# Kernel tuning notes

Hardware: AMD Instinct MI355X
Metric: run time of the kernel (lower is better)

Reference implementation:

```python
import jax, jax.numpy as jnp
import numpy as np

WIN = 5                # win_size
DT = (WIN - 1) // 2    # delta_t
OUT_DIM = 64


def setup_inputs() -> dict:
    key = jax.random.key(0)
    k1, k2, k3 = jax.random.split(key, 3)
    N, C, J, T = 64, 16, 25, 120
    c = C + 1                      # + time channel (signatory.Augment include_time=True)
    sig_ch = c + c * c             # signature_channels(c, depth=2)
    x = jax.random.normal(k1, (N, C, J, T), jnp.float32)
    W = jax.random.normal(k2, (sig_ch, OUT_DIM), jnp.float32) * 0.05
    b = jax.random.normal(k3, (OUT_DIM,), jnp.float32) * 0.05
    return {"x": x, "W": W, "b": b}


def _window_increments(x):
    # Boundary windows are shorter (clip); we emulate them by clipping indices so
    # out-of-range slots duplicate the endpoint -> zero increments -> identity in
    # the tensor algebra, leaving the signature unchanged (faithful to the ragged loop).
    N, C, J, T = x.shape
    t = jnp.arange(T)
    pos = t[:, None] + (jnp.arange(WIN) - DT)[None, :]
    start = jnp.maximum(t - DT, 0)
    end = jnp.minimum(t + DT + 1, T)
    L = (end - start).astype(jnp.float32)                     # window length, >= DT+1
    pc = jnp.clip(pos, 0, T - 1)
    xp = jnp.transpose(x, (0, 2, 3, 1))                       # [N,J,T,C]
    pts = xp[:, :, pc, :]
    # signatory time channel = linspace(0,1,L) over the valid window;
    # duplicated boundary slots share the endpoint's time (zero increment)
    time = (pc - start[:, None]).astype(jnp.float32) / (L[:, None] - 1.0)
    time_b = jnp.broadcast_to(time[None, None, :, :, None], (N, J, T, WIN, 1))
    path = jnp.concatenate([pts, time_b], axis=-1)
    path = jnp.concatenate([jnp.zeros_like(path[..., :1, :]), path], axis=-2)  # basepoint=True
    return jnp.diff(path, axis=-2)


def _signature_depth2(inc):
    c = inc.shape[-1]
    lead = inc.shape[:-2]
    S1 = jnp.zeros(lead + (c,), inc.dtype)
    S2 = jnp.zeros(lead + (c, c), inc.dtype)

    def step(carry, v):
        S1, S2 = carry
        S2 = S2 + S1[..., :, None] * v[..., None, :] + 0.5 * (v[..., :, None] * v[..., None, :])
        S1 = S1 + v
        return (S1, S2), None

    (S1, S2), _ = jax.lax.scan(step, (S1, S2), jnp.moveaxis(inc, -2, 0))
    return S1, S2


def reference(x, W, b):
    inc = _window_increments(x)
    S1, S2 = _signature_depth2(inc)                           # [N,J,T,c], [N,J,T,c,c]
    y = jnp.concatenate([S1, S2.reshape(S2.shape[:-2] + (-1,))], axis=-1)  # [N,J,T,306]
    z = jnp.einsum('njts,so->njto', y, W) + b                 # Linear
    return jnp.transpose(z, (0, 3, 1, 2))                     # [N,out_dim,J,T]
```

## Files before the change

### kernel.cpp

```cpp
#include <hip/hip_runtime.h>
#include <hip/hip_fp16.h>

#define J_DIM 25
#define T_DIM 120
#define O_DIM 64
#define KPAD  328
#define TB    64
#define WROWS 68
#define XPADH 24

typedef _Float16 f16x8 __attribute__((ext_vector_type(8)));
typedef __attribute__((ext_vector_type(4))) float f32x4;

__device__ __forceinline__ unsigned h2bits(__half2 h) {
    unsigned u; __builtin_memcpy(&u, &h, 4); return u;
}
__device__ __forceinline__ __half2 bits2h(unsigned u) {
    __half2 h; __builtin_memcpy(&h, &u, 4); return h;
}
__device__ __forceinline__ __half2 sel4h(int q, __half2 a, __half2 b, __half2 c, __half2 d) {
    unsigned s01 = (q & 1) ? h2bits(b) : h2bits(a);
    unsigned s23 = (q & 1) ? h2bits(d) : h2bits(c);
    return bits2h((q & 2) ? s23 : s01);
}

__global__ void wprep(const float* __restrict__ W, __half* __restrict__ Wf) {
    int i = blockIdx.x * 256 + threadIdx.x;
    if (i >= O_DIM * KPAD) return;
    int o = i / KPAD, k = i % KPAD;
    int a = k / 18, b = k % 18;
    float v = 0.0f;
    if (k < 306) v = (b == 17) ? W[a * O_DIM + o] : 0.5f * W[(17 + 17 * a + b) * O_DIM + o];
    Wf[o * KPAD + k] = __float2half(v);
}

__global__ __launch_bounds__(256, 2) void sig_mfma(
    const float* __restrict__ x, const __half* __restrict__ Wf,
    const float* __restrict__ bias, float* __restrict__ out)
{
    __shared__ __half xs[WROWS][XPADH];
    __shared__ __half ys[TB * KPAD];

    const int tid = threadIdx.x;
    const int bid = blockIdx.x;
    const int half_ = bid & 1;
    const int j = (bid >> 1) % J_DIM;
    const int n = bid / (2 * J_DIM);
    const int t0 = half_ * 56;
    const int wave = tid >> 6, lane = tid & 63;
    const int l15 = lane & 15, l4 = lane >> 4;

    const float* xbase = x + ((size_t)(n * 16) * J_DIM + j) * T_DIM;
    for (int idx = tid; idx < 16 * WROWS; idx += 256) {
        int c = idx / WROWS, i = idx % WROWS;
        int st = min(max(t0 - 2 + i, 0), T_DIM - 1);
        xs[i][c] = __float2half(xbase[(size_t)c * J_DIM * T_DIM + st]);
    }
    if (tid < TB * 3) {
        int r = tid / 3, p = tid % 3;
        *(uint4*)((char*)ys + r * 656 + 608 + p * 16) = uint4{0, 0, 0, 0};
    }
    __syncthreads();

    {
        const int row = tid >> 2, qg = tid & 3;
        const int t = t0 + row;
        const int start = max(t - 2, 0), end = min(t + 3, T_DIM);
        const float inv = 1.0f / (float)(end - start - 1);
        float ptvf[5];
        #pragma unroll
        for (int w = 0; w < 5; ++w) {
            int pcw = min(max(t - 2 + w, 0), T_DIM - 1);
            ptvf[w] = (float)(pcw - start) * inv;
        }
        __half2 ptvb[5];
        #pragma unroll
        for (int w = 0; w < 5; ++w) ptvb[w] = __float2half2_rn(ptvf[w]);

        __half2 xw[5][8];
        #pragma unroll
        for (int w = 0; w < 5; ++w) {
            uint4 lo = *(const uint4*)&xs[row + w][0];
            uint4 hi = *(const uint4*)&xs[row + w][8];
            xw[w][0] = bits2h(lo.x); xw[w][1] = bits2h(lo.y);
            xw[w][2] = bits2h(lo.z); xw[w][3] = bits2h(lo.w);
            xw[w][4] = bits2h(hi.x); xw[w][5] = bits2h(hi.y);
            xw[w][6] = bits2h(hi.z); xw[w][7] = bits2h(hi.w);
        }

        {
            __half2 pr[5];
            #pragma unroll
            for (int w = 0; w < 5; ++w)
                pr[w] = sel4h(qg, xw[w][0], xw[w][1], xw[w][2], xw[w][3]);
            __half2 hp[5];
            hp[0] = __hneg2(pr[1]);
            hp[1] = __hsub2(pr[0], pr[2]);
            hp[2] = __hsub2(pr[1], pr[3]);
            hp[3] = __hsub2(pr[2], pr[4]);
            hp[4] = __hadd2(pr[3], pr[4]);
            __half2 h0b[5], h1b[5];
            #pragma unroll
            for (int w = 0; w < 5; ++w) {
                h0b[w] = __low2half2(hp[w]);
                h1b[w] = __high2half2(hp[w]);
            }
            unsigned u0[9], u1[9];
            #pragma unroll
            for (int b2 = 0; b2 < 8; ++b2) {
                __half2 a0 = __hmul2(h0b[0], xw[0][b2]);
                __half2 a1 = __hmul2(h1b[0], xw[0][b2]);
                #pragma unroll
                for (int w = 1; w < 5; ++w) {
                    a0 = __hfma2(h0b[w], xw[w][b2], a0);
                    a1 = __hfma2(h1b[w], xw[w][b2], a1);
                }
                u0[b2] = h2bits(a0);
                u1[b2] = h2bits(a1);
            }
            {
                __half2 a16 = __hmul2(hp[0], ptvb[0]);
                #pragma unroll
                for (int w = 1; w < 5; ++w) a16 = __hfma2(hp[w], ptvb[w], a16);
                u0[8] = h2bits(__halves2half2(__low2half(a16),  __low2half(pr[4])));
                u1[8] = h2bits(__halves2half2(__high2half(a16), __high2half(pr[4])));
            }
            char* yr = (char*)ys + row * 656 + 72 * qg;
            *(uint2*)(yr +  0) = uint2{u0[0], u0[1]};
            *(uint2*)(yr +  8) = uint2{u0[2], u0[3]};
            *(uint2*)(yr + 16) = uint2{u0[4], u0[5]};
            *(uint2*)(yr + 24) = uint2{u0[6], u0[7]};
            *(uint2*)(yr + 32) = uint2{u0[8], u1[0]};
            *(uint2*)(yr + 40) = uint2{u1[1], u1[2]};
            *(uint2*)(yr + 48) = uint2{u1[3], u1[4]};
            *(uint2*)(yr + 56) = uint2{u1[5], u1[6]};
            *(uint2*)(yr + 64) = uint2{u1[7], u1[8]};
        }

        {
            __half2 pr[5];
            #pragma unroll
            for (int w = 0; w < 5; ++w)
                pr[w] = sel4h(qg, xw[w][4], xw[w][5], xw[w][6], xw[w][7]);
            __half2 hp[5];
            hp[0] = __hneg2(pr[1]);
            hp[1] = __hsub2(pr[0], pr[2]);
            hp[2] = __hsub2(pr[1], pr[3]);
            hp[3] = __hsub2(pr[2], pr[4]);
            hp[4] = __hadd2(pr[3], pr[4]);
            __half2 h0b[5], h1b[5];
            #pragma unroll
            for (int w = 0; w < 5; ++w) {
                h0b[w] = __low2half2(hp[w]);
                h1b[w] = __high2half2(hp[w]);
            }
            unsigned u0[9], u1[9];
            #pragma unroll
            for (int b2 = 0; b2 < 8; ++b2) {
                __half2 a0 = __hmul2(h0b[0], xw[0][b2]);
                __half2 a1 = __hmul2(h1b[0], xw[0][b2]);
                #pragma unroll
                for (int w = 1; w < 5; ++w) {
                    a0 = __hfma2(h0b[w], xw[w][b2], a0);
                    a1 = __hfma2(h1b[w], xw[w][b2], a1);
                }
                u0[b2] = h2bits(a0);
                u1[b2] = h2bits(a1);
            }
            {
                __half2 a16 = __hmul2(hp[0], ptvb[0]);
                #pragma unroll
                for (int w = 1; w < 5; ++w) a16 = __hfma2(hp[w], ptvb[w], a16);
                u0[8] = h2bits(__halves2half2(__low2half(a16),  __low2half(pr[4])));
                u1[8] = h2bits(__halves2half2(__high2half(a16), __high2half(pr[4])));
            }
            char* yr = (char*)ys + row * 656 + 72 * qg + 288;
            *(uint2*)(yr +  0) = uint2{u0[0], u0[1]};
            *(uint2*)(yr +  8) = uint2{u0[2], u0[3]};
            *(uint2*)(yr + 16) = uint2{u0[4], u0[5]};
            *(uint2*)(yr + 24) = uint2{u0[6], u0[7]};
            *(uint2*)(yr + 32) = uint2{u0[8], u1[0]};
            *(uint2*)(yr + 40) = uint2{u1[1], u1[2]};
            *(uint2*)(yr + 48) = uint2{u1[3], u1[4]};
            *(uint2*)(yr + 56) = uint2{u1[5], u1[6]};
            *(uint2*)(yr + 64) = uint2{u1[7], u1[8]};
        }

        if (qg == 0) {
            __half2 htb[5];
            htb[0] = __float2half2_rn(-ptvf[1]);
            htb[1] = __float2half2_rn(ptvf[0] - ptvf[2]);
            htb[2] = __float2half2_rn(ptvf[1] - ptvf[3]);
            htb[3] = __float2half2_rn(ptvf[2] - ptvf[4]);
            htb[4] = __float2half2_rn(ptvf[3] + ptvf[4]);
            unsigned ut[9];
            #pragma unroll
            for (int b2 = 0; b2 < 8; ++b2) {
                __half2 a = __hmul2(htb[0], xw[0][b2]);
                #pragma unroll
                for (int w = 1; w < 5; ++w) a = __hfma2(htb[w], xw[w][b2], a);
                ut[b2] = h2bits(a);
            }
            {
                __half2 a = __hmul2(htb[0], ptvb[0]);
                #pragma unroll
                for (int w = 1; w < 5; ++w) a = __hfma2(htb[w], ptvb[w], a);
                ut[8] = h2bits(__halves2half2(__low2half(a), __float2half(ptvf[4])));
            }
            char* yt = (char*)ys + row * 656 + 576;
            *(uint2*)(yt +  0) = uint2{ut[0], ut[1]};
            *(uint2*)(yt +  8) = uint2{ut[2], ut[3]};
            *(uint2*)(yt + 16) = uint2{ut[4], ut[5]};
            *(uint2*)(yt + 24) = uint2{ut[6], ut[7]};
            *(unsigned*)(yt + 32) = ut[8];
        }
    }
    __syncthreads();

    {
        const float bv = bias[wave * 16 + l15];
        const __half* Bb = Wf + (size_t)(wave * 16 + l15) * KPAD + l4 * 8;
        f16x8 bfrag[10];
        #pragma unroll
        for (int kk = 0; kk < 10; ++kk)
            bfrag[kk] = *(const f16x8*)(Bb + kk * 32);
        #pragma unroll
        for (int mi = 0; mi < 4; ++mi) {
            const char* Ab = (const char*)ys + (mi * 16 + l15) * 656 + l4 * 16;
            f32x4 acc = f32x4{bv, bv, bv, bv};
            #pragma unroll
            for (int kk = 0; kk < 10; ++kk) {
                f16x8 af = *(const f16x8*)(Ab + kk * 64);
                acc = __builtin_amdgcn_mfma_f32_16x16x32_f16(af, bfrag[kk], acc, 0, 0, 0);
            }
            const int tg = t0 + mi * 16 + l4 * 4;
            float* op = out + ((size_t)(n * O_DIM + wave * 16 + l15) * J_DIM + j) * T_DIM + tg;
            *(f32x4*)op = acc;
        }
    }
}

extern "C" void kernel_launch(void* const* d_in, const int* in_sizes, int n_in,
                              void* d_out, int out_size, void* d_ws, size_t ws_size,
                              hipStream_t stream) {
    const float* x = (const float*)d_in[0];
    const float* W = (const float*)d_in[1];
    const float* b = (const float*)d_in[2];
    float* out = (float*)d_out;
    __half* Wf = (__half*)d_ws;

    wprep<<<(O_DIM * KPAD + 255) / 256, 256, 0, stream>>>(W, Wf);
    sig_mfma<<<64 * J_DIM * 2, 256, 0, stream>>>(x, Wf, b, out);
}
```

Before: 39.16 us.

## Make each wave independent with private LDS tiles and wave barriers

Each wave now loads its own 20-row x slice and builds a 16-row signature tile in a private LDS region. The block-wide __syncthreads calls become wave barriers. The MFMA stage is restructured so each wave keeps its A fragments in registers and loops over the four output-column groups, reading W fragments from global memory inside the loop. This removes cross-wave synchronisation and lets waves overlap, but each wave re-reads overlapping x rows and the whole of W.

```diff
diff --git a/kernel.cpp b/kernel.cpp
--- a/kernel.cpp
+++ b/kernel.cpp
@@ -5,8 +5,6 @@
 #define T_DIM 120
 #define O_DIM 64
 #define KPAD  328
-#define TB    64
-#define WROWS 68
 #define XPADH 24
 
 typedef _Float16 f16x8 __attribute__((ext_vector_type(8)));
@@ -38,33 +36,35 @@
     const float* __restrict__ x, const __half* __restrict__ Wf,
     const float* __restrict__ bias, float* __restrict__ out)
 {
-    __shared__ __half xs[WROWS][XPADH];
-    __shared__ __half ys[TB * KPAD];
+    __shared__ __half xs[4][20][XPADH];
+    __shared__ __half ys[4][16 * KPAD];
 
     const int tid = threadIdx.x;
+    const int wave = tid >> 6, lane = tid & 63;
+    const int l15 = lane & 15, l4 = lane >> 4;
     const int bid = blockIdx.x;
     const int half_ = bid & 1;
     const int j = (bid >> 1) % J_DIM;
     const int n = bid / (2 * J_DIM);
-    const int t0 = half_ * 56;
-    const int wave = tid >> 6, lane = tid & 63;
-    const int l15 = lane & 15, l4 = lane >> 4;
+    const int t0w = half_ * 56 + wave * 16;
 
     const float* xbase = x + ((size_t)(n * 16) * J_DIM + j) * T_DIM;
-    for (int idx = tid; idx < 16 * WROWS; idx += 256) {
-        int c = idx / WROWS, i = idx % WROWS;
-        int st = min(max(t0 - 2 + i, 0), T_DIM - 1);
-        xs[i][c] = __float2half(xbase[(size_t)c * J_DIM * T_DIM + st]);
-    }
-    if (tid < TB * 3) {
-        int r = tid / 3, p = tid % 3;
-        *(uint4*)((char*)ys + r * 656 + 608 + p * 16) = uint4{0, 0, 0, 0};
-    }
-    __syncthreads();
+    #pragma unroll
+    for (int k = 0; k < 5; ++k) {
+        int idx = lane + k * 64;
+        int c = idx / 20, i = idx % 20;
+        int st = min(max(t0w - 2 + i, 0), T_DIM - 1);
+        xs[wave][i][c] = __float2half(xbase[(size_t)c * J_DIM * T_DIM + st]);
+    }
+    if (lane < 32) {
+        int r = lane >> 1, p = lane & 1;
+        *(uint4*)((char*)&ys[wave][0] + r * 656 + 608 + p * 16) = uint4{0, 0, 0, 0};
+    }
+    __builtin_amdgcn_wave_barrier();
 
     {
-        const int row = tid >> 2, qg = tid & 3;
-        const int t = t0 + row;
+        const int row = lane >> 2, qg = lane & 3;
+        const int t = t0w + row;
         const int start = max(t - 2, 0), end = min(t + 3, T_DIM);
         const float inv = 1.0f / (float)(end - start - 1);
         float ptvf[5];
@@ -80,8 +80,8 @@
         __half2 xw[5][8];
         #pragma unroll
         for (int w = 0; w < 5; ++w) {
-            uint4 lo = *(const uint4*)&xs[row + w][0];
-            uint4 hi = *(const uint4*)&xs[row + w][8];
+            uint4 lo = *(const uint4*)&xs[wave][row + w][0];
+            uint4 hi = *(const uint4*)&xs[wave][row + w][8];
             xw[w][0] = bits2h(lo.x); xw[w][1] = bits2h(lo.y);
             xw[w][2] = bits2h(lo.z); xw[w][3] = bits2h(lo.w);
             xw[w][4] = bits2h(hi.x); xw[w][5] = bits2h(hi.y);
@@ -125,7 +125,7 @@
                 u0[8] = h2bits(__halves2half2(__low2half(a16),  __low2half(pr[4])));
                 u1[8] = h2bits(__halves2half2(__high2half(a16), __high2half(pr[4])));
             }
-            char* yr = (char*)ys + row * 656 + 72 * qg;
+            char* yr = (char*)&ys[wave][0] + row * 656 + 72 * qg;
             *(uint2*)(yr +  0) = uint2{u0[0], u0[1]};
             *(uint2*)(yr +  8) = uint2{u0[2], u0[3]};
             *(uint2*)(yr + 16) = uint2{u0[4], u0[5]};
@@ -174,7 +174,7 @@
                 u0[8] = h2bits(__halves2half2(__low2half(a16),  __low2half(pr[4])));
                 u1[8] = h2bits(__halves2half2(__high2half(a16), __high2half(pr[4])));
             }
-            char* yr = (char*)ys + row * 656 + 72 * qg + 288;
+            char* yr = (char*)&ys[wave][0] + row * 656 + 72 * qg + 288;
             *(uint2*)(yr +  0) = uint2{u0[0], u0[1]};
             *(uint2*)(yr +  8) = uint2{u0[2], u0[3]};
             *(uint2*)(yr + 16) = uint2{u0[4], u0[5]};
@@ -207,7 +207,7 @@
                 for (int w = 1; w < 5; ++w) a = __hfma2(htb[w], ptvb[w], a);
                 ut[8] = h2bits(__halves2half2(__low2half(a), __float2half(ptvf[4])));
             }
-            char* yt = (char*)ys + row * 656 + 576;
+            char* yt = (char*)&ys[wave][0] + row * 656 + 576;
             *(uint2*)(yt +  0) = uint2{ut[0], ut[1]};
             *(uint2*)(yt +  8) = uint2{ut[2], ut[3]};
             *(uint2*)(yt + 16) = uint2{ut[4], ut[5]};
@@ -215,26 +215,26 @@
             *(unsigned*)(yt + 32) = ut[8];
         }
     }
-    __syncthreads();
+    __builtin_amdgcn_wave_barrier();
 
     {
-        const float bv = bias[wave * 16 + l15];
-        const __half* Bb = Wf + (size_t)(wave * 16 + l15) * KPAD + l4 * 8;
-        f16x8 bfrag[10];
+        const char* Ab = (const char*)&ys[wave][0] + l15 * 656 + l4 * 16;
+        f16x8 af[10];
         #pragma unroll
         for (int kk = 0; kk < 10; ++kk)
-            bfrag[kk] = *(const f16x8*)(Bb + kk * 32);
-        #pragma unroll
-        for (int mi = 0; mi < 4; ++mi) {
-            const char* Ab = (const char*)ys + (mi * 16 + l15) * 656 + l4 * 16;
+            af[kk] = *(const f16x8*)(Ab + kk * 64);
+        const int tg = t0w + l4 * 4;
+        #pragma unroll
+        for (int c = 0; c < 4; ++c) {
+            const __half* Bb = Wf + (size_t)(c * 16 + l15) * KPAD + l4 * 8;
+            const float bv = bias[c * 16 + l15];
             f32x4 acc = f32x4{bv, bv, bv, bv};
             #pragma unroll
             for (int kk = 0; kk < 10; ++kk) {
-                f16x8 af = *(const f16x8*)(Ab + kk * 64);
-                acc = __builtin_amdgcn_mfma_f32_16x16x32_f16(af, bfrag[kk], acc, 0, 0, 0);
-            }
-            const int tg = t0 + mi * 16 + l4 * 4;
-            float* op = out + ((size_t)(n * O_DIM + wave * 16 + l15) * J_DIM + j) * T_DIM + tg;
+                f16x8 bfr = *(const f16x8*)(Bb + kk * 32);
+                acc = __builtin_amdgcn_mfma_f32_16x16x32_f16(af[kk], bfr, acc, 0, 0, 0);
+            }
+            float* op = out + ((size_t)(n * O_DIM + c * 16 + l15) * J_DIM + j) * T_DIM + tg;
             *(f32x4*)op = acc;
         }
     }
```

New measurement: 53.21 us. 35.9% more time.
